# Kernel optimization log

Measured on AMD Instinct MI355X. Metric: run time of the kernel, lower is better.

## Reference

```python
import jax, jax.numpy as jnp
import numpy as np

B, L, D_MODEL, N_HEADS = 2, 2048, 1024, 16
HEAD_DIM = D_MODEL // N_HEADS  # 64
PAD_START = (3 * L) // 4  # last quarter of keys are padding


def _rope_tables(seq_len, dim, base=10000.0, dtype=jnp.float32):
    inv_freq = 1.0 / (base ** (jnp.arange(0, dim, 2, dtype=jnp.float32) / dim))
    t = jnp.arange(seq_len, dtype=jnp.float32)
    freqs = jnp.einsum('i,j->ij', t, inv_freq)  # (L, dim/2)
    return jnp.cos(freqs).astype(dtype), jnp.sin(freqs).astype(dtype)


def _apply_rope(x, cos, sin):
    # x: (B, H, L, D); cos/sin: (L, D/2)
    cos = cos[None, None]
    sin = sin[None, None]
    x_even, x_odd = x[..., 0::2], x[..., 1::2]
    rot_even = x_even * cos - x_odd * sin
    rot_odd = x_even * sin + x_odd * cos
    return jnp.stack((rot_even, rot_odd), axis=-1).reshape(x.shape)


def setup_inputs() -> dict:
    key = jax.random.key(0)
    k_x, k_wqkv, k_bqkv, k_wout, k_bout = jax.random.split(key, 5)
    x = jax.random.normal(k_x, (B, L, D_MODEL), dtype=jnp.float32)
    Wqkv = jax.random.normal(k_wqkv, (3 * D_MODEL, D_MODEL), dtype=jnp.float32) * 0.02
    bqkv = jax.random.normal(k_bqkv, (3 * D_MODEL,), dtype=jnp.float32) * 0.02
    Wout = jax.random.normal(k_wout, (D_MODEL, D_MODEL), dtype=jnp.float32) * 0.02
    bout = jax.random.normal(k_bout, (D_MODEL,), dtype=jnp.float32) * 0.02
    # True = padded position (end of sequence padded)
    pad_mask = jnp.broadcast_to(jnp.arange(L) >= PAD_START, (B, L))
    return {"x": x, "pad_mask": pad_mask, "Wqkv": Wqkv, "bqkv": bqkv, "Wout": Wout, "bout": bout}


def reference(x, pad_mask, Wqkv, bqkv, Wout, bout):
    Bc, Lc, E = x.shape
    H, D = N_HEADS, HEAD_DIM
    qkv = x @ Wqkv.T + bqkv                       # (B, L, 3E)
    qkv = qkv.reshape(Bc, Lc, 3, H, D)
    q = jnp.transpose(qkv[:, :, 0], (0, 2, 1, 3))  # (B, H, L, D)
    k = jnp.transpose(qkv[:, :, 1], (0, 2, 1, 3))
    v = jnp.transpose(qkv[:, :, 2], (0, 2, 1, 3))
    cos, sin = _rope_tables(Lc, D, dtype=x.dtype)
    q = _apply_rope(q, cos, sin)
    k = _apply_rope(k, cos, sin)
    # Mask exactly as the torch module builds it: attn_mask = causal_upper | key_pad,
    # with torch bool-mask semantics (True = allowed to attend).
    causal_upper = jnp.triu(jnp.ones((Lc, Lc), dtype=bool), 1)[None, None]  # (1,1,L,L)
    key_pad = pad_mask[:, None, None, :]                                     # (B,1,1,L)
    allowed = causal_upper | key_pad                                         # (B,1,L,L)
    scale = 1.0 / jnp.sqrt(jnp.asarray(D, dtype=x.dtype))
    scores = jnp.einsum('bhqd,bhkd->bhqk', q, k) * scale
    scores = jnp.where(allowed, scores, -jnp.inf)
    attn = jax.nn.softmax(scores, axis=-1)
    out = jnp.einsum('bhqk,bhkd->bhqd', attn, v)   # (B, H, L, D)
    out = jnp.transpose(out, (0, 2, 1, 3)).reshape(Bc, Lc, E)
    return out @ Wout.T + bout
```

## Files before the change

kernel.cpp:

```cpp
#include <hip/hip_runtime.h>

#define BB 2
#define LL 2048
#define DM 1024
#define NH 16
#define HD 64
#define PAD_START 1536

typedef short bf16x8 __attribute__((ext_vector_type(8)));
typedef float f32x4 __attribute__((ext_vector_type(4)));

#define MFMA_B16(a, b, c) __builtin_amdgcn_mfma_f32_16x16x32_bf16(a, b, c, 0, 0, 0)

#define GLOAD_LDS16(g, l)                                            \
    __builtin_amdgcn_global_load_lds(                                \
        (const __attribute__((address_space(1))) void*)(g),          \
        (__attribute__((address_space(3))) void*)(l), 16, 0, 0)

__device__ __forceinline__ float bf2f(unsigned short u) {
    union { unsigned int i; float f; } v; v.i = ((unsigned int)u) << 16; return v.f;
}
__device__ __forceinline__ unsigned short f2bf(float f) {
    union { float f; unsigned int i; } v; v.f = f;
    unsigned int x = v.i;
    return (unsigned short)((x + 0x7fffu + ((x >> 16) & 1u)) >> 16);
}

__global__ __launch_bounds__(256) void split_kernel(
    const float* __restrict__ X, const float* __restrict__ Wq,
    const float* __restrict__ Wo,
    unsigned short* __restrict__ Xh,
    unsigned short* __restrict__ Wh,
    unsigned short* __restrict__ Woh,
    float* __restrict__ cosT, float* __restrict__ sinT)
{
    if (blockIdx.x >= 8192) {
        const int idx = (blockIdx.x - 8192) * 256 + threadIdx.x;
        const int l = idx >> 5, pp = idx & 31;
        const float LOG2_1E4 = 13.287712379549449f;
        const float invf = exp2f(-((float)pp) * (LOG2_1E4 / 32.0f));
        const float ang = (float)l * invf;
        cosT[idx] = cosf(ang);
        sinT[idx] = sinf(ang);
        return;
    }
    const size_t e = ((size_t)blockIdx.x * 256 + threadIdx.x) * 4;
    const float* src; unsigned short* dh; size_t o;
    if (e < 4194304)      { src = X;  dh = Xh;  o = e; }
    else if (e < 7340032) { src = Wq; dh = Wh;  o = e - 4194304; }
    else                  { src = Wo; dh = Woh; o = e - 7340032; }
    float4 v = *(const float4*)(src + o);
    ushort4 hv;
    hv.x = f2bf(v.x); hv.y = f2bf(v.y);
    hv.z = f2bf(v.z); hv.w = f2bf(v.w);
    *(ushort4*)(dh + o) = hv;
}

#define ACC_PARAMS f32x4& c00, f32x4& c01, f32x4& c02, f32x4& c03, \
                   f32x4& c10, f32x4& c11, f32x4& c12, f32x4& c13, \
                   f32x4& c20, f32x4& c21, f32x4& c22, f32x4& c23, \
                   f32x4& c30, f32x4& c31, f32x4& c32, f32x4& c33
#define ACC_ARGS c00, c01, c02, c03, c10, c11, c12, c13, \
                 c20, c21, c22, c23, c30, c31, c32, c33

__device__ __forceinline__ void gemm_bk64(
    const unsigned short* __restrict__ A, const unsigned short* __restrict__ B,
    int m0, int n0, unsigned short* As, unsigned short* Bs, ACC_PARAMS)
{
    const int t = threadIdx.x;
    const int lane = t & 63;
    const int w = t >> 6;
    const int wm = (w >> 1) << 6;
    const int wn = (w & 1) << 6;
    const int lm = lane & 15;
    const int quad = lane >> 4;

    const int rop = lane >> 3;
    const int sw  = ((lane & 7) ^ rop) * 8;
    const unsigned short* ga = A + (size_t)(m0 + w * 32 + rop) * 1024 + sw;
    const unsigned short* gb = B + (size_t)(n0 + w * 32 + rop) * 1024 + sw;
    unsigned short* lA0 = As + (w * 32) * 64;
    unsigned short* lB0 = Bs + (w * 32) * 64;

    const int o1 = (quad ^ (lm & 7)) * 8;
    const int o2 = ((quad + 4) ^ (lm & 7)) * 8;
    const int arow = (wm + lm) * 64;
    const int brow = (wn + lm) * 64;

#define STAGE64(bufofs, k0)                                               \
    do {                                                                  \
        GLOAD_LDS16(ga + (k0),             lA0 + (bufofs));               \
        GLOAD_LDS16(ga + (k0) +  8 * 1024, lA0 + (bufofs) +  8 * 64);     \
        GLOAD_LDS16(ga + (k0) + 16 * 1024, lA0 + (bufofs) + 16 * 64);     \
        GLOAD_LDS16(ga + (k0) + 24 * 1024, lA0 + (bufofs) + 24 * 64);     \
        GLOAD_LDS16(gb + (k0),             lB0 + (bufofs));               \
        GLOAD_LDS16(gb + (k0) +  8 * 1024, lB0 + (bufofs) +  8 * 64);     \
        GLOAD_LDS16(gb + (k0) + 16 * 1024, lB0 + (bufofs) + 16 * 64);     \
        GLOAD_LDS16(gb + (k0) + 24 * 1024, lB0 + (bufofs) + 24 * 64);     \
    } while (0)

#define GEMM_HALF(as_, bs_, oo)                                           \
    do {                                                                  \
        bf16x8 a0 = *(const bf16x8*)((as_) + arow +  0 * 64 + (oo));      \
        bf16x8 a1 = *(const bf16x8*)((as_) + arow + 16 * 64 + (oo));      \
        bf16x8 a2 = *(const bf16x8*)((as_) + arow + 32 * 64 + (oo));      \
        bf16x8 a3 = *(const bf16x8*)((as_) + arow + 48 * 64 + (oo));      \
        bf16x8 b0 = *(const bf16x8*)((bs_) + brow +  0 * 64 + (oo));      \
        bf16x8 b1 = *(const bf16x8*)((bs_) + brow + 16 * 64 + (oo));      \
        bf16x8 b2 = *(const bf16x8*)((bs_) + brow + 32 * 64 + (oo));      \
        bf16x8 b3 = *(const bf16x8*)((bs_) + brow + 48 * 64 + (oo));      \
        c00 = MFMA_B16(a0, b0, c00); c01 = MFMA_B16(a0, b1, c01);         \
        c02 = MFMA_B16(a0, b2, c02); c03 = MFMA_B16(a0, b3, c03);         \
        c10 = MFMA_B16(a1, b0, c10); c11 = MFMA_B16(a1, b1, c11);         \
        c12 = MFMA_B16(a1, b2, c12); c13 = MFMA_B16(a1, b3, c13);         \
        c20 = MFMA_B16(a2, b0, c20); c21 = MFMA_B16(a2, b1, c21);         \
        c22 = MFMA_B16(a2, b2, c22); c23 = MFMA_B16(a2, b3, c23);         \
        c30 = MFMA_B16(a3, b0, c30); c31 = MFMA_B16(a3, b1, c31);         \
        c32 = MFMA_B16(a3, b2, c32); c33 = MFMA_B16(a3, b3, c33);         \
    } while (0)

    STAGE64(0, 0);
    __syncthreads();

    for (int k0 = 0; k0 < 1024; k0 += 128) {
        STAGE64(8192, k0 + 64);
        GEMM_HALF(As, Bs, o1);
        GEMM_HALF(As, Bs, o2);
        __syncthreads();
        if (k0 + 128 < 1024) STAGE64(0, k0 + 128);
        GEMM_HALF(As + 8192, Bs + 8192, o1);
        GEMM_HALF(As + 8192, Bs + 8192, o2);
        __syncthreads();
    }
#undef STAGE64
#undef GEMM_HALF
}

__device__ __forceinline__ void qk_frag(
    f32x4 cf, int r0, int bh, int d, float bv, float qscale,
    const float* __restrict__ cosT, const float* __restrict__ sinT,
    unsigned short* __restrict__ dst, bool odd)
{
    const int p = d >> 1;
#pragma unroll
    for (int e = 0; e < 4; ++e) {
        const int l = (r0 + e) & (LL - 1);
        const float x = cf[e] + bv;
        const float px = __shfl_xor(x, 1);
        const float cs = cosT[l * 32 + p];
        const float sn = sinT[l * 32 + p];
        const float ve = odd ? px : x;
        const float vo = odd ? x : px;
        float res = odd ? (ve * sn + vo * cs) : (ve * cs - vo * sn);
        res *= qscale;
        const float other = __shfl_xor(res, 1);
        if (!odd) {
            const unsigned int pk = ((unsigned int)f2bf(res)) |
                                    (((unsigned int)f2bf(other)) << 16);
            *(unsigned int*)(dst + ((size_t)bh * LL + l) * HD + d) = pk;
        }
    }
}

__device__ __forceinline__ void v_frag(
    f32x4 cf, int l0, int bh, int d, float bv, unsigned short* __restrict__ vt)
{
    ushort4 pk;
    pk.x = f2bf(cf[0] + bv); pk.y = f2bf(cf[1] + bv);
    pk.z = f2bf(cf[2] + bv); pk.w = f2bf(cf[3] + bv);
    *(ushort4*)(vt + ((size_t)(bh * HD + d)) * LL + l0) = pk;
}

__device__ __forceinline__ void out_frag(
    f32x4 cf, int r0, int c, float bv, float* __restrict__ C)
{
#pragma unroll
    for (int e = 0; e < 4; ++e)
        C[(size_t)(r0 + e) * DM + c] = cf[e] + bv;
}

__global__ __launch_bounds__(256) void qkv_mfma(
    const unsigned short* __restrict__ Xh,
    const unsigned short* __restrict__ Wh,
    const float* __restrict__ bias,
    const float* __restrict__ cosT, const float* __restrict__ sinT,
    unsigned short* __restrict__ qs, unsigned short* __restrict__ ks,
    unsigned short* __restrict__ vt)
{
    __shared__ unsigned short As[2 * 128 * 64];
    __shared__ unsigned short Bs[2 * 128 * 64];
    const int bid = blockIdx.y * 24 + blockIdx.x;
    const int swz = (bid & 7) * 96 + (bid >> 3);
    const int n0 = (swz % 24) * 128;
    const int m0 = (swz / 24) * 128;
    f32x4 c00 = {0,0,0,0}, c01 = {0,0,0,0}, c02 = {0,0,0,0}, c03 = {0,0,0,0};
    f32x4 c10 = {0,0,0,0}, c11 = {0,0,0,0}, c12 = {0,0,0,0}, c13 = {0,0,0,0};
    f32x4 c20 = {0,0,0,0}, c21 = {0,0,0,0}, c22 = {0,0,0,0}, c23 = {0,0,0,0};
    f32x4 c30 = {0,0,0,0}, c31 = {0,0,0,0}, c32 = {0,0,0,0}, c33 = {0,0,0,0};

    gemm_bk64(Xh, Wh, m0, n0, As, Bs, ACC_ARGS);

    const int t = threadIdx.x;
    const int lane = t & 63;
    const int w = t >> 6;
    const int wm = (w >> 1) << 6;
    const int wn = (w & 1) << 6;
    const int lm = lane & 15;
    const int quad = lane >> 4;

    const int s = n0 >> 10;
    const int cb = n0 + wn;
    const int h = (cb >> 6) & (NH - 1);
    const int bi = m0 >> 11;
    const int bh = bi * NH + h;
    const int rbase = m0 + wm;

    if (s == 2) {
#define VSTORE(rt, ct) \
        v_frag(c##rt##ct, (rbase + rt * 16 + quad * 4) & (LL - 1), bh, \
               ct * 16 + lm, bias[cb + ct * 16 + lm], vt);
        VSTORE(0,0) VSTORE(0,1) VSTORE(0,2) VSTORE(0,3)
        VSTORE(1,0) VSTORE(1,1) VSTORE(1,2) VSTORE(1,3)
        VSTORE(2,0) VSTORE(2,1) VSTORE(2,2) VSTORE(2,3)
        VSTORE(3,0) VSTORE(3,1) VSTORE(3,2) VSTORE(3,3)
#undef VSTORE
    } else {
        unsigned short* dst = (s == 0) ? qs : ks;
        const float qscale = (s == 0) ? 0.125f : 1.0f;
        const bool odd = (lm & 1) != 0;
#define QKSTORE(rt, ct) \
        qk_frag(c##rt##ct, rbase + rt * 16 + quad * 4, bh, ct * 16 + lm, \
                bias[cb + ct * 16 + lm], qscale, cosT, sinT, dst, odd);
        QKSTORE(0,0) QKSTORE(0,1) QKSTORE(0,2) QKSTORE(0,3)
        QKSTORE(1,0) QKSTORE(1,1) QKSTORE(1,2) QKSTORE(1,3)
        QKSTORE(2,0) QKSTORE(2,1) QKSTORE(2,2) QKSTORE(2,3)
        QKSTORE(3,0) QKSTORE(3,1) QKSTORE(3,2) QKSTORE(3,3)
#undef QKSTORE
    }
}

__global__ __launch_bounds__(256) void attn_mfma(
    const unsigned short* __restrict__ qs,
    const unsigned short* __restrict__ ks,
    const unsigned short* __restrict__ vt,
    unsigned short* __restrict__ aoh)
{
    __shared__ unsigned short Ks[64 * 72];
    __shared__ unsigned short Vs[64 * 72];
    __shared__ unsigned short Pl[4][16 * 72];

    const int bh = blockIdx.y;
    const int qt = (blockIdx.x + blockIdx.y) & 31;
    const int q0 = qt * 64;
    const int b = bh >> 4, h = bh & (NH - 1);
    const int tid = threadIdx.x;
    const int w = tid >> 6;
    const int lane = tid & 63;
    const int lm = lane & 15;
    const int quad = lane >> 4;
    const int qw0 = q0 + w * 16;

    const unsigned short* qbase = qs + ((size_t)bh * LL + qw0 + lm) * HD + quad * 8;
    const bf16x8 qf0 = *(const bf16x8*)(qbase);
    const bf16x8 qf1 = *(const bf16x8*)(qbase + 32);

    f32x4 O[4];
#pragma unroll
    for (int dd = 0; dd < 4; ++dd) O[dd] = (f32x4){0.f, 0.f, 0.f, 0.f};
    float lrow[4] = {0.f, 0.f, 0.f, 0.f};

    const unsigned short* kbase = ks + (size_t)bh * LL * HD;
    const unsigned short* vtb   = vt + (size_t)bh * HD * LL;
    unsigned short* pw = &Pl[w][0];

    const int srow = tid >> 3;
    const int sch  = (tid & 7) * 8;

    const int t0 = ((q0 < PAD_START) ? q0 : PAD_START) >> 6;

    int k0 = t0 * 64;
    uint4 ka0 = *(const uint4*)(kbase + (size_t)(k0 + srow) * HD + sch);
    uint4 ka1 = *(const uint4*)(kbase + (size_t)(k0 + srow + 32) * HD + sch);
    uint4 va0 = *(const uint4*)(vtb + (size_t)srow * LL + k0 + sch);
    uint4 va1 = *(const uint4*)(vtb + (size_t)(srow + 32) * LL + k0 + sch);

    for (int tt = t0; tt < 32; ++tt) {
        k0 = tt * 64;
        __syncthreads();
        *(uint4*)(Ks + srow * 72 + sch)        = ka0;
        *(uint4*)(Ks + (srow + 32) * 72 + sch) = ka1;
        *(uint4*)(Vs + srow * 72 + sch)        = va0;
        *(uint4*)(Vs + (srow + 32) * 72 + sch) = va1;
        __syncthreads();

        {
            const int kn = ((tt + 1) < 32 ? (tt + 1) : 31) * 64;
            ka0 = *(const uint4*)(kbase + (size_t)(kn + srow) * HD + sch);
            ka1 = *(const uint4*)(kbase + (size_t)(kn + srow + 32) * HD + sch);
            va0 = *(const uint4*)(vtb + (size_t)srow * LL + kn + sch);
            va1 = *(const uint4*)(vtb + (size_t)(srow + 32) * LL + kn + sch);
        }

        f32x4 sfrag[4];
#pragma unroll
        for (int c = 0; c < 4; ++c) {
            const bf16x8 kf0 = *(const bf16x8*)(Ks + (c * 16 + lm) * 72 + quad * 8);
            const bf16x8 kf1 = *(const bf16x8*)(Ks + (c * 16 + lm) * 72 + 32 + quad * 8);
            f32x4 z = (f32x4){0.f, 0.f, 0.f, 0.f};
            z = MFMA_B16(qf0, kf0, z);
            z = MFMA_B16(qf1, kf1, z);
            sfrag[c] = z;
        }
        if (tt == t0 && q0 < PAD_START) {
#pragma unroll
            for (int c = 0; c < 4; ++c) {
                const int kg = k0 + c * 16 + lm;
#pragma unroll
                for (int r = 0; r < 4; ++r) {
                    const int qg = qw0 + quad * 4 + r;
                    if (kg <= qg) sfrag[c][r] = -1e30f;
                }
            }
        }
#pragma unroll
        for (int r = 0; r < 4; ++r) {
#pragma unroll
            for (int c = 0; c < 4; ++c) {
                const float p = __expf(sfrag[c][r]);
                lrow[r] += p;
                pw[(quad * 4 + r) * 72 + c * 16 + lm] = f2bf(p);
            }
        }
        const bf16x8 a0 = *(const bf16x8*)(pw + lm * 72 + quad * 8);
        const bf16x8 a1 = *(const bf16x8*)(pw + lm * 72 + 32 + quad * 8);
#pragma unroll
        for (int dd = 0; dd < 4; ++dd) {
            const bf16x8 b0 = *(const bf16x8*)(Vs + (dd * 16 + lm) * 72 + quad * 8);
            const bf16x8 b1 = *(const bf16x8*)(Vs + (dd * 16 + lm) * 72 + 32 + quad * 8);
            O[dd] = MFMA_B16(a0, b0, O[dd]);
            O[dd] = MFMA_B16(a1, b1, O[dd]);
        }
    }

#pragma unroll
    for (int r = 0; r < 4; ++r) {
        float rs = lrow[r];
        rs += __shfl_xor(rs, 1);
        rs += __shfl_xor(rs, 2);
        rs += __shfl_xor(rs, 4);
        rs += __shfl_xor(rs, 8);
        lrow[r] = rs;
    }

#pragma unroll
    for (int r = 0; r < 4; ++r) {
        const float inv = 1.0f / lrow[r];
        const int qg = qw0 + quad * 4 + r;
        const size_t base = ((size_t)(b * LL + qg)) * DM + h * HD;
#pragma unroll
        for (int dd = 0; dd < 4; ++dd)
            aoh[base + dd * 16 + lm] = f2bf(O[dd][r] * inv);
    }
}

__global__ __launch_bounds__(256) void out_mfma(
    const unsigned short* __restrict__ Ah,
    const unsigned short* __restrict__ Wh,
    const float* __restrict__ bias, float* __restrict__ C)
{
    __shared__ unsigned short As[2 * 128 * 64];
    __shared__ unsigned short Bs[2 * 128 * 64];
    const int bid = blockIdx.y * 8 + blockIdx.x;
    const int swz = (bid & 7) * 32 + (bid >> 3);
    const int n0 = (swz % 8) * 128;
    const int m0 = (swz / 8) * 128;

    f32x4 c00 = {0,0,0,0}, c01 = {0,0,0,0}, c02 = {0,0,0,0}, c03 = {0,0,0,0};
    f32x4 c10 = {0,0,0,0}, c11 = {0,0,0,0}, c12 = {0,0,0,0}, c13 = {0,0,0,0};
    f32x4 c20 = {0,0,0,0}, c21 = {0,0,0,0}, c22 = {0,0,0,0}, c23 = {0,0,0,0};
    f32x4 c30 = {0,0,0,0}, c31 = {0,0,0,0}, c32 = {0,0,0,0}, c33 = {0,0,0,0};

    gemm_bk64(Ah, Wh, m0, n0, As, Bs, ACC_ARGS);

    const int t = threadIdx.x;
    const int lane = t & 63;
    const int w = t >> 6;
    const int wm = (w >> 1) << 6;
    const int wn = (w & 1) << 6;
    const int lm = lane & 15;
    const int quad = lane >> 4;

#define CSTORE(rt, ct) \
    out_frag(c##rt##ct, m0 + wm + rt * 16 + quad * 4, \
             n0 + wn + ct * 16 + lm, bias[n0 + wn + ct * 16 + lm], C);
    CSTORE(0,0) CSTORE(0,1) CSTORE(0,2) CSTORE(0,3)
    CSTORE(1,0) CSTORE(1,1) CSTORE(1,2) CSTORE(1,3)
    CSTORE(2,0) CSTORE(2,1) CSTORE(2,2) CSTORE(2,3)
    CSTORE(3,0) CSTORE(3,1) CSTORE(3,2) CSTORE(3,3)
#undef CSTORE
}

extern "C" void kernel_launch(void* const* d_in, const int* in_sizes, int n_in,
                              void* d_out, int out_size, void* d_ws, size_t ws_size,
                              hipStream_t stream)
{
    const float* x    = (const float*)d_in[0];
    const float* Wqkv = (const float*)d_in[2];
    const float* bqkv = (const float*)d_in[3];
    const float* Wout = (const float*)d_in[4];
    const float* bout = (const float*)d_in[5];
    float* out = (float*)d_out;

    unsigned short* p = (unsigned short*)d_ws;
    const size_t SZ = (size_t)BB * NH * LL * HD;
    unsigned short* qsb = p; p += SZ;
    unsigned short* ksb = p; p += SZ;
    unsigned short* vtb = p; p += SZ;
    unsigned short* Xhi = p; p += SZ;
    unsigned short* Whi = p; p += (size_t)3145728;
    unsigned short* Wohi = p; p += (size_t)1048576;
    float* cosT = (float*)p; p += (size_t)2 * 65536;
    float* sinT = (float*)p; p += (size_t)2 * 65536;

    split_kernel<<<8448, 256, 0, stream>>>(x, Wqkv, Wout,
                                           Xhi, Whi, Wohi, cosT, sinT);
    dim3 g1(24, 32);
    qkv_mfma<<<g1, 256, 0, stream>>>(Xhi, Whi, bqkv, cosT, sinT,
                                     qsb, ksb, vtb);
    dim3 g2(32, 32);
    attn_mfma<<<g2, 256, 0, stream>>>(qsb, ksb, vtb, Xhi);
    dim3 g3(8, 32);
    out_mfma<<<g3, 256, 0, stream>>>(Xhi, Wohi, bout, out);
}
```

Baseline: 225.7 us.

## Use 256x256 GEMM tiles with 8 waves and explicit barrier/waitcnt pipelining

```diff
diff --git a/kernel.cpp b/kernel.cpp
--- a/kernel.cpp
+++ b/kernel.cpp
@@ -56,22 +56,16 @@
     *(ushort4*)(dh + o) = hv;
 }
 
-#define ACC_PARAMS f32x4& c00, f32x4& c01, f32x4& c02, f32x4& c03, \
-                   f32x4& c10, f32x4& c11, f32x4& c12, f32x4& c13, \
-                   f32x4& c20, f32x4& c21, f32x4& c22, f32x4& c23, \
-                   f32x4& c30, f32x4& c31, f32x4& c32, f32x4& c33
-#define ACC_ARGS c00, c01, c02, c03, c10, c11, c12, c13, \
-                 c20, c21, c22, c23, c30, c31, c32, c33
-
-__device__ __forceinline__ void gemm_bk64(
+__device__ __forceinline__ void gemm256(
     const unsigned short* __restrict__ A, const unsigned short* __restrict__ B,
-    int m0, int n0, unsigned short* As, unsigned short* Bs, ACC_PARAMS)
+    int m0, int n0, unsigned short* As, unsigned short* Bs,
+    f32x4 (&acc)[8][4])
 {
     const int t = threadIdx.x;
     const int lane = t & 63;
     const int w = t >> 6;
-    const int wm = (w >> 1) << 6;
-    const int wn = (w & 1) << 6;
+    const int wm = w >> 2;
+    const int wn = w & 3;
     const int lm = lane & 15;
     const int quad = lane >> 4;
 
@@ -79,61 +73,75 @@
     const int sw  = ((lane & 7) ^ rop) * 8;
     const unsigned short* ga = A + (size_t)(m0 + w * 32 + rop) * 1024 + sw;
     const unsigned short* gb = B + (size_t)(n0 + w * 32 + rop) * 1024 + sw;
-    unsigned short* lA0 = As + (w * 32) * 64;
-    unsigned short* lB0 = Bs + (w * 32) * 64;
+    unsigned short* lA = As + (w * 32) * 64;
+    unsigned short* lB = Bs + (w * 32) * 64;
 
     const int o1 = (quad ^ (lm & 7)) * 8;
     const int o2 = ((quad + 4) ^ (lm & 7)) * 8;
-    const int arow = (wm + lm) * 64;
-    const int brow = (wn + lm) * 64;
-
-#define STAGE64(bufofs, k0)                                               \
+    const int ar = (wm * 128 + lm) * 64;
+    const int br = (wn * 64 + lm) * 64;
+
+#define STG256(bo, k0)                                                    \
     do {                                                                  \
-        GLOAD_LDS16(ga + (k0),             lA0 + (bufofs));               \
-        GLOAD_LDS16(ga + (k0) +  8 * 1024, lA0 + (bufofs) +  8 * 64);     \
-        GLOAD_LDS16(ga + (k0) + 16 * 1024, lA0 + (bufofs) + 16 * 64);     \
-        GLOAD_LDS16(ga + (k0) + 24 * 1024, lA0 + (bufofs) + 24 * 64);     \
-        GLOAD_LDS16(gb + (k0),             lB0 + (bufofs));               \
-        GLOAD_LDS16(gb + (k0) +  8 * 1024, lB0 + (bufofs) +  8 * 64);     \
-        GLOAD_LDS16(gb + (k0) + 16 * 1024, lB0 + (bufofs) + 16 * 64);     \
-        GLOAD_LDS16(gb + (k0) + 24 * 1024, lB0 + (bufofs) + 24 * 64);     \
+        GLOAD_LDS16(ga + (k0),             lA + (bo));                    \
+        GLOAD_LDS16(ga + (k0) +  8 * 1024, lA + (bo) +  8 * 64);          \
+        GLOAD_LDS16(ga + (k0) + 16 * 1024, lA + (bo) + 16 * 64);          \
+        GLOAD_LDS16(ga + (k0) + 24 * 1024, lA + (bo) + 24 * 64);          \
+        GLOAD_LDS16(gb + (k0),             lB + (bo));                    \
+        GLOAD_LDS16(gb + (k0) +  8 * 1024, lB + (bo) +  8 * 64);          \
+        GLOAD_LDS16(gb + (k0) + 16 * 1024, lB + (bo) + 16 * 64);          \
+        GLOAD_LDS16(gb + (k0) + 24 * 1024, lB + (bo) + 24 * 64);          \
     } while (0)
 
-#define GEMM_HALF(as_, bs_, oo)                                           \
+#define TILE256(bo, do_stage, kstage, vmN)                                \
     do {                                                                  \
-        bf16x8 a0 = *(const bf16x8*)((as_) + arow +  0 * 64 + (oo));      \
-        bf16x8 a1 = *(const bf16x8*)((as_) + arow + 16 * 64 + (oo));      \
-        bf16x8 a2 = *(const bf16x8*)((as_) + arow + 32 * 64 + (oo));      \
-        bf16x8 a3 = *(const bf16x8*)((as_) + arow + 48 * 64 + (oo));      \
-        bf16x8 b0 = *(const bf16x8*)((bs_) + brow +  0 * 64 + (oo));      \
-        bf16x8 b1 = *(const bf16x8*)((bs_) + brow + 16 * 64 + (oo));      \
-        bf16x8 b2 = *(const bf16x8*)((bs_) + brow + 32 * 64 + (oo));      \
-        bf16x8 b3 = *(const bf16x8*)((bs_) + brow + 48 * 64 + (oo));      \
-        c00 = MFMA_B16(a0, b0, c00); c01 = MFMA_B16(a0, b1, c01);         \
-        c02 = MFMA_B16(a0, b2, c02); c03 = MFMA_B16(a0, b3, c03);         \
-        c10 = MFMA_B16(a1, b0, c10); c11 = MFMA_B16(a1, b1, c11);         \
-        c12 = MFMA_B16(a1, b2, c12); c13 = MFMA_B16(a1, b3, c13);         \
-        c20 = MFMA_B16(a2, b0, c20); c21 = MFMA_B16(a2, b1, c21);         \
-        c22 = MFMA_B16(a2, b2, c22); c23 = MFMA_B16(a2, b3, c23);         \
-        c30 = MFMA_B16(a3, b0, c30); c31 = MFMA_B16(a3, b1, c31);         \
-        c32 = MFMA_B16(a3, b2, c32); c33 = MFMA_B16(a3, b3, c33);         \
+        bf16x8 af[8][2]; bf16x8 bfr[4][2];                                \
+        _Pragma("unroll")                                                 \
+        for (int mf = 0; mf < 8; ++mf) {                                  \
+            af[mf][0] = *(const bf16x8*)(As + (bo) + ar + mf * 1024 + o1);\
+            af[mf][1] = *(const bf16x8*)(As + (bo) + ar + mf * 1024 + o2);\
+        }                                                                 \
+        _Pragma("unroll")                                                 \
+        for (int nf = 0; nf < 4; ++nf) {                                  \
+            bfr[nf][0] = *(const bf16x8*)(Bs + (bo) + br + nf * 1024 + o1);\
+            bfr[nf][1] = *(const bf16x8*)(Bs + (bo) + br + nf * 1024 + o2);\
+        }                                                                 \
+        asm volatile("s_waitcnt lgkmcnt(0)" ::: "memory");                \
+        __builtin_amdgcn_sched_barrier(0);                                \
+        __builtin_amdgcn_s_barrier();          \
+        __builtin_amdgcn_sched_barrier(0);                                \
+        if (do_stage) { STG256(bo, kstage); }                             \
+        asm volatile("s_waitcnt vmcnt(" #vmN ")" ::: "memory");           \
+        __builtin_amdgcn_sched_barrier(0);                                \
+        __builtin_amdgcn_s_barrier();       \
+        __builtin_amdgcn_sched_barrier(0);                                \
+        __builtin_amdgcn_s_setprio(1);                                    \
+        _Pragma("unroll")                                                 \
+        for (int mf = 0; mf < 8; ++mf) {                                  \
+            _Pragma("unroll")                                             \
+            for (int nf = 0; nf < 4; ++nf) {                              \
+                acc[mf][nf] = MFMA_B16(af[mf][0], bfr[nf][0], acc[mf][nf]);\
+                acc[mf][nf] = MFMA_B16(af[mf][1], bfr[nf][1], acc[mf][nf]);\
+            }                                                             \
+        }                                                                 \
+        __builtin_amdgcn_s_setprio(0);                                    \
     } while (0)
 
-    STAGE64(0, 0);
-    __syncthreads();
-
-    for (int k0 = 0; k0 < 1024; k0 += 128) {
-        STAGE64(8192, k0 + 64);
-        GEMM_HALF(As, Bs, o1);
-        GEMM_HALF(As, Bs, o2);
-        __syncthreads();
-        if (k0 + 128 < 1024) STAGE64(0, k0 + 128);
-        GEMM_HALF(As + 8192, Bs + 8192, o1);
-        GEMM_HALF(As + 8192, Bs + 8192, o2);
-        __syncthreads();
-    }
-#undef STAGE64
-#undef GEMM_HALF
+    STG256(0, 0);
+    STG256(16384, 64);
+    asm volatile("s_waitcnt vmcnt(8)" ::: "memory");
+    __builtin_amdgcn_sched_barrier(0);
+    __builtin_amdgcn_s_barrier();
+    __builtin_amdgcn_sched_barrier(0);
+
+    for (int k0 = 0; k0 < 896; k0 += 128) {
+        TILE256(0,     1, k0 + 128, 8);
+        TILE256(16384, 1, k0 + 192, 8);
+    }
+    TILE256(0,     0, 0, 0);
+    TILE256(16384, 0, 0, 0);
+#undef TILE256
+#undef STG256
 }
 
 __device__ __forceinline__ void qk_frag(
@@ -179,7 +187,7 @@
         C[(size_t)(r0 + e) * DM + c] = cf[e] + bv;
 }
 
-__global__ __launch_bounds__(256) void qkv_mfma(
+__global__ __launch_bounds__(512) void qkv_mfma(
     const unsigned short* __restrict__ Xh,
     const unsigned short* __restrict__ Wh,
     const float* __restrict__ bias,
@@ -187,55 +195,57 @@
     unsigned short* __restrict__ qs, unsigned short* __restrict__ ks,
     unsigned short* __restrict__ vt)
 {
-    __shared__ unsigned short As[2 * 128 * 64];
-    __shared__ unsigned short Bs[2 * 128 * 64];
-    const int bid = blockIdx.y * 24 + blockIdx.x;
-    const int swz = (bid & 7) * 96 + (bid >> 3);
-    const int n0 = (swz % 24) * 128;
-    const int m0 = (swz / 24) * 128;
-    f32x4 c00 = {0,0,0,0}, c01 = {0,0,0,0}, c02 = {0,0,0,0}, c03 = {0,0,0,0};
-    f32x4 c10 = {0,0,0,0}, c11 = {0,0,0,0}, c12 = {0,0,0,0}, c13 = {0,0,0,0};
-    f32x4 c20 = {0,0,0,0}, c21 = {0,0,0,0}, c22 = {0,0,0,0}, c23 = {0,0,0,0};
-    f32x4 c30 = {0,0,0,0}, c31 = {0,0,0,0}, c32 = {0,0,0,0}, c33 = {0,0,0,0};
-
-    gemm_bk64(Xh, Wh, m0, n0, As, Bs, ACC_ARGS);
+    __shared__ unsigned short As[2 * 256 * 64];
+    __shared__ unsigned short Bs[2 * 256 * 64];
+
+    const int bid = blockIdx.y * 12 + blockIdx.x;
+    const int xcd = bid & 7;
+    const int i   = bid >> 3;
+    const int mt  = (xcd & 3) * 4 + (i & 3);
+    const int nt  = (xcd >> 2) * 6 + (i >> 2);
+    const int m0 = mt * 256, n0 = nt * 256;
+
+    f32x4 acc[8][4];
+#pragma unroll
+    for (int mf = 0; mf < 8; ++mf)
+#pragma unroll
+        for (int nf = 0; nf < 4; ++nf) acc[mf][nf] = (f32x4){0.f,0.f,0.f,0.f};
+
+    gemm256(Xh, Wh, m0, n0, As, Bs, acc);
 
     const int t = threadIdx.x;
     const int lane = t & 63;
     const int w = t >> 6;
-    const int wm = (w >> 1) << 6;
-    const int wn = (w & 1) << 6;
+    const int wm = w >> 2;
+    const int wn = w & 3;
     const int lm = lane & 15;
     const int quad = lane >> 4;
 
     const int s = n0 >> 10;
-    const int cb = n0 + wn;
-    const int h = (cb >> 6) & (NH - 1);
+    const int cbw = n0 + wn * 64;
+    const int h = (cbw >> 6) & (NH - 1);
     const int bi = m0 >> 11;
     const int bh = bi * NH + h;
-    const int rbase = m0 + wm;
+    const int rbase = m0 + wm * 128;
 
     if (s == 2) {
-#define VSTORE(rt, ct) \
-        v_frag(c##rt##ct, (rbase + rt * 16 + quad * 4) & (LL - 1), bh, \
-               ct * 16 + lm, bias[cb + ct * 16 + lm], vt);
-        VSTORE(0,0) VSTORE(0,1) VSTORE(0,2) VSTORE(0,3)
-        VSTORE(1,0) VSTORE(1,1) VSTORE(1,2) VSTORE(1,3)
-        VSTORE(2,0) VSTORE(2,1) VSTORE(2,2) VSTORE(2,3)
-        VSTORE(3,0) VSTORE(3,1) VSTORE(3,2) VSTORE(3,3)
-#undef VSTORE
+#pragma unroll
+        for (int mf = 0; mf < 8; ++mf)
+#pragma unroll
+            for (int nf = 0; nf < 4; ++nf)
+                v_frag(acc[mf][nf], (rbase + mf * 16 + quad * 4) & (LL - 1), bh,
+                       nf * 16 + lm, bias[cbw + nf * 16 + lm], vt);
     } else {
         unsigned short* dst = (s == 0) ? qs : ks;
         const float qscale = (s == 0) ? 0.125f : 1.0f;
         const bool odd = (lm & 1) != 0;
-#define QKSTORE(rt, ct) \
-        qk_frag(c##rt##ct, rbase + rt * 16 + quad * 4, bh, ct * 16 + lm, \
-                bias[cb + ct * 16 + lm], qscale, cosT, sinT, dst, odd);
-        QKSTORE(0,0) QKSTORE(0,1) QKSTORE(0,2) QKSTORE(0,3)
-        QKSTORE(1,0) QKSTORE(1,1) QKSTORE(1,2) QKSTORE(1,3)
-        QKSTORE(2,0) QKSTORE(2,1) QKSTORE(2,2) QKSTORE(2,3)
-        QKSTORE(3,0) QKSTORE(3,1) QKSTORE(3,2) QKSTORE(3,3)
-#undef QKSTORE
+#pragma unroll
+        for (int mf = 0; mf < 8; ++mf)
+#pragma unroll
+            for (int nf = 0; nf < 4; ++nf)
+                qk_frag(acc[mf][nf], rbase + mf * 16 + quad * 4, bh,
+                        nf * 16 + lm, bias[cbw + nf * 16 + lm], qscale,
+                        cosT, sinT, dst, odd);
     }
 }
 
@@ -363,41 +373,44 @@
     }
 }
 
-__global__ __launch_bounds__(256) void out_mfma(
+__global__ __launch_bounds__(512) void out_mfma(
     const unsigned short* __restrict__ Ah,
     const unsigned short* __restrict__ Wh,
     const float* __restrict__ bias, float* __restrict__ C)
 {
-    __shared__ unsigned short As[2 * 128 * 64];
-    __shared__ unsigned short Bs[2 * 128 * 64];
-    const int bid = blockIdx.y * 8 + blockIdx.x;
-    const int swz = (bid & 7) * 32 + (bid >> 3);
-    const int n0 = (swz % 8) * 128;
-    const int m0 = (swz / 8) * 128;
-
-    f32x4 c00 = {0,0,0,0}, c01 = {0,0,0,0}, c02 = {0,0,0,0}, c03 = {0,0,0,0};
-    f32x4 c10 = {0,0,0,0}, c11 = {0,0,0,0}, c12 = {0,0,0,0}, c13 = {0,0,0,0};
-    f32x4 c20 = {0,0,0,0}, c21 = {0,0,0,0}, c22 = {0,0,0,0}, c23 = {0,0,0,0};
-    f32x4 c30 = {0,0,0,0}, c31 = {0,0,0,0}, c32 = {0,0,0,0}, c33 = {0,0,0,0};
-
-    gemm_bk64(Ah, Wh, m0, n0, As, Bs, ACC_ARGS);
+    __shared__ unsigned short As[2 * 256 * 64];
+    __shared__ unsigned short Bs[2 * 256 * 64];
+
+    const int bid = blockIdx.y * 4 + blockIdx.x;
+    const int xcd = bid & 7;
+    const int i   = bid >> 3;
+    const int mt  = xcd * 2 + (i & 1);
+    const int nt  = i >> 1;
+    const int m0 = mt * 256, n0 = nt * 256;
+
+    f32x4 acc[8][4];
+#pragma unroll
+    for (int mf = 0; mf < 8; ++mf)
+#pragma unroll
+        for (int nf = 0; nf < 4; ++nf) acc[mf][nf] = (f32x4){0.f,0.f,0.f,0.f};
+
+    gemm256(Ah, Wh, m0, n0, As, Bs, acc);
 
     const int t = threadIdx.x;
     const int lane = t & 63;
     const int w = t >> 6;
-    const int wm = (w >> 1) << 6;
-    const int wn = (w & 1) << 6;
+    const int wm = w >> 2;
+    const int wn = w & 3;
     const int lm = lane & 15;
     const int quad = lane >> 4;
 
-#define CSTORE(rt, ct) \
-    out_frag(c##rt##ct, m0 + wm + rt * 16 + quad * 4, \
-             n0 + wn + ct * 16 + lm, bias[n0 + wn + ct * 16 + lm], C);
-    CSTORE(0,0) CSTORE(0,1) CSTORE(0,2) CSTORE(0,3)
-    CSTORE(1,0) CSTORE(1,1) CSTORE(1,2) CSTORE(1,3)
-    CSTORE(2,0) CSTORE(2,1) CSTORE(2,2) CSTORE(2,3)
-    CSTORE(3,0) CSTORE(3,1) CSTORE(3,2) CSTORE(3,3)
-#undef CSTORE
+#pragma unroll
+    for (int mf = 0; mf < 8; ++mf)
+#pragma unroll
+        for (int nf = 0; nf < 4; ++nf)
+            out_frag(acc[mf][nf], m0 + wm * 128 + mf * 16 + quad * 4,
+                     n0 + wn * 64 + nf * 16 + lm,
+                     bias[n0 + wn * 64 + nf * 16 + lm], C);
 }
 
 extern "C" void kernel_launch(void* const* d_in, const int* in_sizes, int n_in,
@@ -424,11 +437,11 @@
 
     split_kernel<<<8448, 256, 0, stream>>>(x, Wqkv, Wout,
                                            Xhi, Whi, Wohi, cosT, sinT);
-    dim3 g1(24, 32);
-    qkv_mfma<<<g1, 256, 0, stream>>>(Xhi, Whi, bqkv, cosT, sinT,
+    dim3 g1(12, 16);
+    qkv_mfma<<<g1, 512, 0, stream>>>(Xhi, Whi, bqkv, cosT, sinT,
                                      qsb, ksb, vtb);
     dim3 g2(32, 32);
     attn_mfma<<<g2, 256, 0, stream>>>(qsb, ksb, vtb, Xhi);
-    dim3 g3(8, 32);
-    out_mfma<<<g3, 256, 0, stream>>>(Xhi, Wohi, bout, out);
-}
+    dim3 g3(4, 16);
+    out_mfma<<<g3, 512, 0, stream>>>(Xhi, Wohi, bout, out);
+}
```

Result: no change. 228.6 us (+1.3%).

## Use 256x256 tiles with 8-wave pipelined MFMA GEMM for QKV projection

Applied to the files above, without the earlier changes.

```diff
diff --git a/kernel.cpp b/kernel.cpp
--- a/kernel.cpp
+++ b/kernel.cpp
@@ -54,6 +54,132 @@
     hv.x = f2bf(v.x); hv.y = f2bf(v.y);
     hv.z = f2bf(v.z); hv.w = f2bf(v.w);
     *(ushort4*)(dh + o) = hv;
+}
+
+__device__ __forceinline__ void gemm256(
+    const unsigned short* __restrict__ A, const unsigned short* __restrict__ B,
+    int m0, int n0, unsigned short* As, unsigned short* Bs,
+    f32x4 (&acc)[8][4])
+{
+    const int t = threadIdx.x;
+    const int lane = t & 63;
+    const int w = t >> 6;
+    const int wm = w >> 2;
+    const int wn = w & 3;
+    const int lm = lane & 15;
+    const int quad = lane >> 4;
+
+    const int rop = lane >> 3;
+    const int sw  = ((lane & 7) ^ rop) * 8;
+    const unsigned short* ga = A + (size_t)(m0 + w * 32 + rop) * 1024 + sw;
+    const unsigned short* gb = B + (size_t)(n0 + w * 32 + rop) * 1024 + sw;
+    unsigned short* lA = As + (w * 32) * 64;
+    unsigned short* lB = Bs + (w * 32) * 64;
+
+    const int o1 = (quad ^ (lm & 7)) * 8;
+    const int o2 = ((quad + 4) ^ (lm & 7)) * 8;
+    const int ar = (wm * 128 + lm) * 64;
+    const int br = (wn * 64 + lm) * 64;
+
+#define LDSB16(p) (*(const bf16x8*)(p))
+
+#define STG_A2(BO2, KA, R0, R1)                                           \
+    do {                                                                  \
+        GLOAD_LDS16(ga + (KA) + (R0) * 1024, lA + (BO2) + (R0) * 64);     \
+        GLOAD_LDS16(ga + (KA) + (R1) * 1024, lA + (BO2) + (R1) * 64);     \
+    } while (0)
+#define STG_B2(BOB, KB, R0, R1)                                           \
+    do {                                                                  \
+        GLOAD_LDS16(gb + (KB) + (R0) * 1024, lB + (BOB) + (R0) * 64);     \
+        GLOAD_LDS16(gb + (KB) + (R1) * 1024, lB + (BOB) + (R1) * 64);     \
+    } while (0)
+
+#define PHASE_TAIL(MFA, MFB)                                              \
+    __builtin_amdgcn_s_barrier();                                         \
+    asm volatile("s_waitcnt lgkmcnt(0)" ::: "memory");                    \
+    __builtin_amdgcn_sched_barrier(0);                                    \
+    __builtin_amdgcn_s_setprio(1);                                        \
+    _Pragma("unroll")                                                     \
+    for (int nf = 0; nf < 4; ++nf) {                                      \
+        acc[MFA][nf] = MFMA_B16(aA[0], bf_[nf][0], acc[MFA][nf]);         \
+        acc[MFA][nf] = MFMA_B16(aA[1], bf_[nf][1], acc[MFA][nf]);         \
+        acc[MFB][nf] = MFMA_B16(aB[0], bf_[nf][0], acc[MFB][nf]);         \
+        acc[MFB][nf] = MFMA_B16(aB[1], bf_[nf][1], acc[MFB][nf]);         \
+    }                                                                     \
+    __builtin_amdgcn_s_setprio(0);                                        \
+    __builtin_amdgcn_s_barrier();
+
+#define TILE8(BO, BO2, SA, KA, SB, KB, DR, VMN)                           \
+    {                                                                     \
+        bf16x8 bf_[4][2];                                                 \
+        {             \
+            _Pragma("unroll")                                             \
+            for (int nf = 0; nf < 4; ++nf) {                              \
+                bf_[nf][0] = LDSB16(Bs + (BO) + br + nf * 1024 + o1);     \
+                bf_[nf][1] = LDSB16(Bs + (BO) + br + nf * 1024 + o2);     \
+            }                                                             \
+            bf16x8 aA[2], aB[2];                                          \
+            aA[0] = LDSB16(As + (BO) + ar + 0 * 1024 + o1);               \
+            aA[1] = LDSB16(As + (BO) + ar + 0 * 1024 + o2);               \
+            aB[0] = LDSB16(As + (BO) + ar + 1 * 1024 + o1);               \
+            aB[1] = LDSB16(As + (BO) + ar + 1 * 1024 + o2);               \
+            if (SA) { STG_A2(BO2, KA, 0, 8); }                            \
+            asm volatile("s_waitcnt lgkmcnt(8)" ::: "memory");            \
+            PHASE_TAIL(0, 1)                                              \
+        }                                                                 \
+        {                                      \
+            bf16x8 aA[2], aB[2];                                          \
+            aA[0] = LDSB16(As + (BO) + ar + 2 * 1024 + o1);               \
+            aA[1] = LDSB16(As + (BO) + ar + 2 * 1024 + o2);               \
+            aB[0] = LDSB16(As + (BO) + ar + 3 * 1024 + o1);               \
+            aB[1] = LDSB16(As + (BO) + ar + 3 * 1024 + o2);               \
+            if (SA) { STG_A2(BO2, KA, 16, 24); }                          \
+            PHASE_TAIL(2, 3)                                              \
+        }                                                                 \
+        {                                      \
+            bf16x8 aA[2], aB[2];                                          \
+            aA[0] = LDSB16(As + (BO) + ar + 4 * 1024 + o1);               \
+            aA[1] = LDSB16(As + (BO) + ar + 4 * 1024 + o2);               \
+            aB[0] = LDSB16(As + (BO) + ar + 5 * 1024 + o1);               \
+            aB[1] = LDSB16(As + (BO) + ar + 5 * 1024 + o2);               \
+            if (SB) { STG_B2(BO, KB, 0, 8); }                             \
+            PHASE_TAIL(4, 5)                                              \
+        }                                                                 \
+        {                      \
+            bf16x8 aA[2], aB[2];                                          \
+            aA[0] = LDSB16(As + (BO) + ar + 6 * 1024 + o1);               \
+            aA[1] = LDSB16(As + (BO) + ar + 6 * 1024 + o2);               \
+            aB[0] = LDSB16(As + (BO) + ar + 7 * 1024 + o1);               \
+            aB[1] = LDSB16(As + (BO) + ar + 7 * 1024 + o2);               \
+            if (SB) { STG_B2(BO, KB, 16, 24); }                           \
+            if (DR) {                                                     \
+                asm volatile("s_waitcnt vmcnt(" VMN ")" ::: "memory");    \
+                __builtin_amdgcn_sched_barrier(0);                        \
+            }                                                             \
+            PHASE_TAIL(6, 7)                                              \
+        }                                                                 \
+    }
+
+    STG_A2(0, 0, 0, 8);   STG_A2(0, 0, 16, 24);
+    STG_B2(0, 0, 0, 8);   STG_B2(0, 0, 16, 24);
+    STG_B2(16384, 64, 0, 8); STG_B2(16384, 64, 16, 24);
+    asm volatile("s_waitcnt vmcnt(4)" ::: "memory");
+    __builtin_amdgcn_sched_barrier(0);
+    __builtin_amdgcn_s_barrier();
+
+    for (int t2 = 0; t2 < 7; ++t2) {
+        const int k = t2 * 128;
+        TILE8(0,     16384, 1, k + 64,  1, k + 128, 1, "4")
+        TILE8(16384, 0,     1, k + 128, 1, k + 192, 1, "4")
+    }
+    TILE8(0,     16384, 1, 960, 0, 0, 1, "0")
+    TILE8(16384, 0,     0, 0,   0, 0, 0, "0")
+
+#undef TILE8
+#undef PHASE_TAIL
+#undef STG_B2
+#undef STG_A2
+#undef LDSB16
 }
 
 #define ACC_PARAMS f32x4& c00, f32x4& c01, f32x4& c02, f32x4& c03, \
@@ -179,7 +305,7 @@
         C[(size_t)(r0 + e) * DM + c] = cf[e] + bv;
 }
 
-__global__ __launch_bounds__(256) void qkv_mfma(
+__global__ __launch_bounds__(512) void qkv_mfma(
     const unsigned short* __restrict__ Xh,
     const unsigned short* __restrict__ Wh,
     const float* __restrict__ bias,
@@ -187,55 +313,57 @@
     unsigned short* __restrict__ qs, unsigned short* __restrict__ ks,
     unsigned short* __restrict__ vt)
 {
-    __shared__ unsigned short As[2 * 128 * 64];
-    __shared__ unsigned short Bs[2 * 128 * 64];
-    const int bid = blockIdx.y * 24 + blockIdx.x;
-    const int swz = (bid & 7) * 96 + (bid >> 3);
-    const int n0 = (swz % 24) * 128;
-    const int m0 = (swz / 24) * 128;
-    f32x4 c00 = {0,0,0,0}, c01 = {0,0,0,0}, c02 = {0,0,0,0}, c03 = {0,0,0,0};
-    f32x4 c10 = {0,0,0,0}, c11 = {0,0,0,0}, c12 = {0,0,0,0}, c13 = {0,0,0,0};
-    f32x4 c20 = {0,0,0,0}, c21 = {0,0,0,0}, c22 = {0,0,0,0}, c23 = {0,0,0,0};
-    f32x4 c30 = {0,0,0,0}, c31 = {0,0,0,0}, c32 = {0,0,0,0}, c33 = {0,0,0,0};
-
-    gemm_bk64(Xh, Wh, m0, n0, As, Bs, ACC_ARGS);
+    __shared__ unsigned short As[2 * 256 * 64];
+    __shared__ unsigned short Bs[2 * 256 * 64];
+
+    const int bid = blockIdx.y * 12 + blockIdx.x;
+    const int xcd = bid & 7;
+    const int i   = bid >> 3;
+    const int mt  = (xcd & 3) * 4 + (i & 3);
+    const int nt  = (xcd >> 2) * 6 + (i >> 2);
+    const int m0 = mt * 256, n0 = nt * 256;
+
+    f32x4 acc[8][4];
+#pragma unroll
+    for (int mf = 0; mf < 8; ++mf)
+#pragma unroll
+        for (int nf = 0; nf < 4; ++nf) acc[mf][nf] = (f32x4){0.f,0.f,0.f,0.f};
+
+    gemm256(Xh, Wh, m0, n0, As, Bs, acc);
 
     const int t = threadIdx.x;
     const int lane = t & 63;
     const int w = t >> 6;
-    const int wm = (w >> 1) << 6;
-    const int wn = (w & 1) << 6;
+    const int wm = w >> 2;
+    const int wn = w & 3;
     const int lm = lane & 15;
     const int quad = lane >> 4;
 
     const int s = n0 >> 10;
-    const int cb = n0 + wn;
-    const int h = (cb >> 6) & (NH - 1);
+    const int cbw = n0 + wn * 64;
+    const int h = (cbw >> 6) & (NH - 1);
     const int bi = m0 >> 11;
     const int bh = bi * NH + h;
-    const int rbase = m0 + wm;
+    const int rbase = m0 + wm * 128;
 
     if (s == 2) {
-#define VSTORE(rt, ct) \
-        v_frag(c##rt##ct, (rbase + rt * 16 + quad * 4) & (LL - 1), bh, \
-               ct * 16 + lm, bias[cb + ct * 16 + lm], vt);
-        VSTORE(0,0) VSTORE(0,1) VSTORE(0,2) VSTORE(0,3)
-        VSTORE(1,0) VSTORE(1,1) VSTORE(1,2) VSTORE(1,3)
-        VSTORE(2,0) VSTORE(2,1) VSTORE(2,2) VSTORE(2,3)
-        VSTORE(3,0) VSTORE(3,1) VSTORE(3,2) VSTORE(3,3)
-#undef VSTORE
+#pragma unroll
+        for (int mf = 0; mf < 8; ++mf)
+#pragma unroll
+            for (int nf = 0; nf < 4; ++nf)
+                v_frag(acc[mf][nf], (rbase + mf * 16 + quad * 4) & (LL - 1), bh,
+                       nf * 16 + lm, bias[cbw + nf * 16 + lm], vt);
     } else {
         unsigned short* dst = (s == 0) ? qs : ks;
         const float qscale = (s == 0) ? 0.125f : 1.0f;
         const bool odd = (lm & 1) != 0;
-#define QKSTORE(rt, ct) \
-        qk_frag(c##rt##ct, rbase + rt * 16 + quad * 4, bh, ct * 16 + lm, \
-                bias[cb + ct * 16 + lm], qscale, cosT, sinT, dst, odd);
-        QKSTORE(0,0) QKSTORE(0,1) QKSTORE(0,2) QKSTORE(0,3)
-        QKSTORE(1,0) QKSTORE(1,1) QKSTORE(1,2) QKSTORE(1,3)
-        QKSTORE(2,0) QKSTORE(2,1) QKSTORE(2,2) QKSTORE(2,3)
-        QKSTORE(3,0) QKSTORE(3,1) QKSTORE(3,2) QKSTORE(3,3)
-#undef QKSTORE
+#pragma unroll
+        for (int mf = 0; mf < 8; ++mf)
+#pragma unroll
+            for (int nf = 0; nf < 4; ++nf)
+                qk_frag(acc[mf][nf], rbase + mf * 16 + quad * 4, bh,
+                        nf * 16 + lm, bias[cbw + nf * 16 + lm], qscale,
+                        cosT, sinT, dst, odd);
     }
 }
 
@@ -370,10 +498,8 @@
 {
     __shared__ unsigned short As[2 * 128 * 64];
     __shared__ unsigned short Bs[2 * 128 * 64];
-    const int bid = blockIdx.y * 8 + blockIdx.x;
-    const int swz = (bid & 7) * 32 + (bid >> 3);
-    const int n0 = (swz % 8) * 128;
-    const int m0 = (swz / 8) * 128;
+    const int n0 = blockIdx.x * 128;
+    const int m0 = blockIdx.y * 128;
 
     f32x4 c00 = {0,0,0,0}, c01 = {0,0,0,0}, c02 = {0,0,0,0}, c03 = {0,0,0,0};
     f32x4 c10 = {0,0,0,0}, c11 = {0,0,0,0}, c12 = {0,0,0,0}, c13 = {0,0,0,0};
@@ -424,8 +550,8 @@
 
     split_kernel<<<8448, 256, 0, stream>>>(x, Wqkv, Wout,
                                            Xhi, Whi, Wohi, cosT, sinT);
-    dim3 g1(24, 32);
-    qkv_mfma<<<g1, 256, 0, stream>>>(Xhi, Whi, bqkv, cosT, sinT,
+    dim3 g1(12, 16);
+    qkv_mfma<<<g1, 512, 0, stream>>>(Xhi, Whi, bqkv, cosT, sinT,
                                      qsb, ksb, vtb);
     dim3 g2(32, 32);
     attn_mfma<<<g2, 256, 0, stream>>>(qsb, ksb, vtb, Xhi);
```

New measurement: 226.7 us. No clear change (+0.4%).
